# Kernel tuning notes

Measured on AMD Instinct MI355X. Metric: run time of the kernel, lower is better.

## Reference

```python
import jax, jax.numpy as jnp
import numpy as np


def setup_inputs() -> dict:
    key = jax.random.key(0)
    kH, kU, kW = jax.random.split(key, 3)
    T, J, D2 = 16384, 1024, 512  # T x 2d context, J x 2d query
    H = jax.random.normal(kH, (T, D2), dtype=jnp.float32)
    U = jax.random.normal(kU, (J, D2), dtype=jnp.float32)
    Ws = jax.random.normal(kW, (3 * D2, 1), dtype=jnp.float32) * 0.05
    return {"H": H, "U": U, "Ws": Ws}


def reference(H, U, Ws):
    D2 = H.shape[-1]
    # Ws applied to concat([H_dup, U_dup, H_dup*U_dup]) decomposes into three blocks.
    w1 = Ws[:D2, 0]          # (2d,)
    w2 = Ws[D2:2 * D2, 0]    # (2d,)
    w3 = Ws[2 * D2:, 0]      # (2d,)
    # Trilinear similarity S[t, j] = H[t]@w1 + U[j]@w2 + (H[t]*U[j])@w3  -> (T, J)
    S = (H @ w1)[:, None] + (U @ w2)[None, :] + (H * w3) @ U.T
    # C2Q attention: softmax over query axis, attend query vectors -> (T, 2d)
    attended_query = jax.nn.softmax(S, axis=-1) @ U
    # Q2C attention: softmax over T of max_j S, rank-1 summary of context -> (2d,)
    b = jax.nn.softmax(jnp.max(S, axis=-1))
    h_tilde = b @ H  # (2d,), tiled to (T, 2d) by broadcasting
    # Merge to query-aware representation G -> (T, 8d)
    G = jnp.concatenate(
        [H, attended_query, H * attended_query, H * h_tilde[None, :]], axis=-1
    )
    return G
```

## Files before the change

### kernel.cpp

```cpp
#include <hip/hip_runtime.h>
#include <hip/hip_bf16.h>

#define T_ROWS 16384
#define J_DIM  1024
#define D_DIM  512

typedef __attribute__((ext_vector_type(8))) short bf16x8;
typedef __attribute__((ext_vector_type(4))) float f32x4;
typedef unsigned short u16;

__device__ __forceinline__ u16 f2bf(float f) {
    union { float f; unsigned int u; } v; v.f = f;
    return (u16)((v.u + 0x7FFFu + ((v.u >> 16) & 1u)) >> 16);
}
__device__ __forceinline__ float bf2f(u16 b) {
    union { unsigned int u; float f; } v; v.u = ((unsigned int)b) << 16;
    return v.f;
}

__device__ __forceinline__ void gload16(const void* g, void* l) {
    __builtin_amdgcn_global_load_lds(
        (__attribute__((address_space(1))) void*)(unsigned long long)(size_t)g,
        (__attribute__((address_space(3))) void*)(unsigned int)(size_t)l,
        16, 0, 0);
}

template<int NT>
__device__ __forceinline__ void gemm_core(
    const u16* A, int lda, const u16* B, int ldb, u16* lds, f32x4 (&acc)[4][4])
{
    const int tid  = threadIdx.x;
    const int lane = tid & 63;
    const int w    = tid >> 6;
    const int wr   = w >> 1, wc = w & 1;
    const int fr   = lane & 15, quad = lane >> 4;

    const int srow = tid >> 2;
    const int ss   = (tid & 3) ^ ((srow >> 1) & 3);

    const u16* gA0 = A + (size_t)srow * lda + ss * 8;
    const u16* gA1 = A + (size_t)(srow + 64) * lda + ss * 8;
    const u16* gB0 = B + (size_t)srow * ldb + ss * 8;
    const u16* gB1 = B + (size_t)(srow + 64) * ldb + ss * 8;

    u16* As = lds;
    u16* Bs = lds + 8192;
    u16* dA0 = As + tid * 8;
    u16* dA1 = As + 2048 + tid * 8;
    u16* dB0 = Bs + tid * 8;
    u16* dB1 = Bs + 2048 + tid * 8;

    gload16(gA0, dA0); gload16(gA1, dA1);
    gload16(gB0, dB0); gload16(gB1, dB1);
    gA0 += 32; gA1 += 32; gB0 += 32; gB1 += 32;

    int offA[4], offB[4];
    #pragma unroll
    for (int i = 0; i < 4; ++i) {
        const int rA = wr * 64 + i * 16 + fr;
        offA[i] = rA * 32 + (quad ^ ((rA >> 1) & 3)) * 8;
        const int rB = wc * 64 + i * 16 + fr;
        offB[i] = rB * 32 + (quad ^ ((rB >> 1) & 3)) * 8;
    }
    __syncthreads();

    #pragma unroll 2
    for (int t = 0; t < NT; ++t) {
        const int cur = (t & 1) * 4096;
        const int nxt = 4096 - cur;
        if (t + 1 < NT) {
            gload16(gA0, dA0 + nxt); gload16(gA1, dA1 + nxt);
            gload16(gB0, dB0 + nxt); gload16(gB1, dB1 + nxt);
            gA0 += 32; gA1 += 32; gB0 += 32; gB1 += 32;
        }
        const u16* Ac = As + cur;
        const u16* Bc = Bs + cur;
        bf16x8 af[4], bfr[4];
        #pragma unroll
        for (int i = 0; i < 4; ++i) af[i]  = *(const bf16x8*)(Ac + offA[i]);
        #pragma unroll
        for (int i = 0; i < 4; ++i) bfr[i] = *(const bf16x8*)(Bc + offB[i]);
        #pragma unroll
        for (int mf = 0; mf < 4; ++mf)
            #pragma unroll
            for (int nf = 0; nf < 4; ++nf)
                acc[mf][nf] = __builtin_amdgcn_mfma_f32_16x16x32_bf16(
                    af[mf], bfr[nf], acc[mf][nf], 0, 0, 0);
        __syncthreads();
    }
}

__global__ __launch_bounds__(128) void prep_u(
    const float* __restrict__ U, const float* __restrict__ Ws,
    float* __restrict__ uw2, u16* __restrict__ Ub, u16* __restrict__ Utp)
{
    const int j = blockIdx.x;
    const int t = threadIdx.x;
    const float4 u  = ((const float4*)(U + (size_t)j * D_DIM))[t];
    const float4 w2 = ((const float4*)(Ws + D_DIM))[t];
    float p = u.x * w2.x + u.y * w2.y + u.z * w2.z + u.w * w2.w;
    #pragma unroll
    for (int m = 1; m < 64; m <<= 1) p += __shfl_xor(p, m);
    __shared__ float red[2];
    if ((t & 63) == 0) red[t >> 6] = p;
    __syncthreads();
    if (t == 0) uw2[j] = red[0] + red[1];

    ushort4 v;
    v.x = f2bf(u.x); v.y = f2bf(u.y); v.z = f2bf(u.z); v.w = f2bf(u.w);
    ((ushort4*)(Ub + (size_t)j * D_DIM))[t] = v;

    const size_t jpart = (size_t)(j >> 5) * 512 + (size_t)(((j >> 3) & 3) * 128) + (j & 7);
    const u16 bs[4] = { v.x, v.y, v.z, v.w };
    #pragma unroll
    for (int s = 0; s < 4; ++s) {
        const int d = 4 * t + s;
        Utp[(size_t)(d >> 4) * 16384 + jpart + (size_t)(d & 15) * 8] = bs[s];
    }
}

__global__ __launch_bounds__(128) void prep_h(
    const float* __restrict__ H, const float* __restrict__ Ws,
    float* __restrict__ hw1, u16* outU)
{
    const int i = blockIdx.x;
    const int t = threadIdx.x;
    const float4 h  = ((const float4*)(H + (size_t)i * D_DIM))[t];
    const float4 w1 = ((const float4*)Ws)[t];
    const float4 w3 = ((const float4*)(Ws + 2 * D_DIM))[t];
    float p = h.x * w1.x + h.y * w1.y + h.z * w1.z + h.w * w1.w;
    #pragma unroll
    for (int m = 1; m < 64; m <<= 1) p += __shfl_xor(p, m);
    __shared__ float red[2];
    if ((t & 63) == 0) red[t >> 6] = p;
    __syncthreads();
    if (t == 0) hw1[i] = red[0] + red[1];

    ushort4 q;
    q.x = f2bf(h.x * w3.x); q.y = f2bf(h.y * w3.y);
    q.z = f2bf(h.z * w3.z); q.w = f2bf(h.w * w3.w);
    *(ushort4*)(outU + (size_t)i * 4096 + 3072 + 4 * t) = q;
}

__global__ __launch_bounds__(256) void s_gemm(
    u16* outU, const u16* __restrict__ Ub, const float* __restrict__ uw2,
    float* __restrict__ pmax)
{
    __shared__ u16 lds[16384];
    const int bid = blockIdx.x;
    const int swz = (bid & 7) * 128 + (bid >> 3);
    const int bm = swz >> 3, nb = swz & 7;

    f32x4 acc[4][4];
    #pragma unroll
    for (int i = 0; i < 4; ++i)
        #pragma unroll
        for (int j = 0; j < 4; ++j) acc[i][j] = (f32x4){0.f, 0.f, 0.f, 0.f};

    gemm_core<16>(outU + (size_t)bm * 128 * 4096 + 3072, 4096,
                  Ub + (size_t)nb * 128 * 512, 512, lds, acc);

    const int tid = threadIdx.x, lane = tid & 63, w = tid >> 6;
    const int wr = w >> 1, wc = w & 1, fr = lane & 15, quad = lane >> 4;
    int jc[4]; float u2[4];
    #pragma unroll
    for (int nf = 0; nf < 4; ++nf) {
        jc[nf] = nb * 128 + wc * 64 + nf * 16 + fr;
        u2[nf] = uw2[jc[nf]];
    }
    float* redf = (float*)lds;
    #pragma unroll
    for (int mf = 0; mf < 4; ++mf)
        #pragma unroll
        for (int m = 0; m < 4; ++m) {
            float mv = -1e30f;
            #pragma unroll
            for (int nf = 0; nf < 4; ++nf) {
                acc[mf][nf][m] += u2[nf];
                mv = fmaxf(mv, acc[mf][nf][m]);
            }
            mv = fmaxf(mv, __shfl_xor(mv, 1));
            mv = fmaxf(mv, __shfl_xor(mv, 2));
            mv = fmaxf(mv, __shfl_xor(mv, 4));
            mv = fmaxf(mv, __shfl_xor(mv, 8));
            if (fr == 0) redf[wc * 128 + wr * 64 + mf * 16 + quad * 4 + m] = mv;
        }
    __syncthreads();
    if (wc == 0 && fr == 0) {
        #pragma unroll
        for (int mf = 0; mf < 4; ++mf)
            #pragma unroll
            for (int m = 0; m < 4; ++m) {
                const int rr = wr * 64 + mf * 16 + quad * 4 + m;
                pmax[((size_t)bm * 128 + rr) * 8 + nb] =
                    fmaxf(redf[rr], redf[128 + rr]);
            }
    }
    #pragma unroll
    for (int mf = 0; mf < 4; ++mf)
        #pragma unroll
        for (int m = 0; m < 4; ++m) {
            const size_t row = (size_t)bm * 128 + wr * 64 + mf * 16 + quad * 4 + m;
            u16* rp = outU + row * 4096 + 1024;
            #pragma unroll
            for (int nf = 0; nf < 4; ++nf) rp[jc[nf]] = f2bf(acc[mf][nf][m]);
        }
}

__global__ __launch_bounds__(1024) void bsoft2(
    const float* __restrict__ pmax, const float* __restrict__ hw1,
    float* __restrict__ bvec)
{
    __shared__ float red[16];
    __shared__ float Msh, Lsh;
    const int t = threadIdx.x;
    float rs[16];
    #pragma unroll
    for (int e = 0; e < 16; ++e) {
        const int r = t + e * 1024;
        const float4 p0 = *(const float4*)(pmax + (size_t)r * 8);
        const float4 p1 = *(const float4*)(pmax + (size_t)r * 8 + 4);
        rs[e] = fmaxf(fmaxf(fmaxf(p0.x, p0.y), fmaxf(p0.z, p0.w)),
                      fmaxf(fmaxf(p1.x, p1.y), fmaxf(p1.z, p1.w))) + hw1[r];
    }
    float m = -1e30f;
    #pragma unroll
    for (int e = 0; e < 16; ++e) m = fmaxf(m, rs[e]);
    #pragma unroll
    for (int s = 1; s < 64; s <<= 1) m = fmaxf(m, __shfl_xor(m, s));
    if ((t & 63) == 0) red[t >> 6] = m;
    __syncthreads();
    if (t == 0) {
        float M = red[0];
        for (int i = 1; i < 16; ++i) M = fmaxf(M, red[i]);
        Msh = M;
    }
    __syncthreads();
    const float M = Msh;
    float l = 0.f;
    #pragma unroll
    for (int e = 0; e < 16; ++e) l += __expf(rs[e] - M);
    #pragma unroll
    for (int s = 1; s < 64; s <<= 1) l += __shfl_xor(l, s);
    if ((t & 63) == 0) red[t >> 6] = l;
    __syncthreads();
    if (t == 0) {
        float L = 0.f;
        for (int i = 0; i < 16; ++i) L += red[i];
        Lsh = L;
    }
    __syncthreads();
    const float invL = 1.f / Lsh;
    #pragma unroll
    for (int e = 0; e < 16; ++e) bvec[t + e * 1024] = __expf(rs[e] - M) * invL;
}

__global__ __launch_bounds__(512) void htilde_partial(
    const float* __restrict__ H, const float* __restrict__ b,
    float* __restrict__ part)
{
    const int blk = blockIdx.x;
    const int d = threadIdx.x;
    const int i0 = blk * 64;
    float s = 0.f;
    for (int rI = 0; rI < 64; ++rI)
        s += b[i0 + rI] * H[(size_t)(i0 + rI) * D_DIM + d];
    part[(size_t)blk * D_DIM + d] = s;
}

__global__ __launch_bounds__(512) void htilde_reduce(
    const float* __restrict__ part, float* __restrict__ ht)
{
    const int d = threadIdx.x;
    float s = 0.f;
    for (int p = 0; p < 256; ++p) s += part[(size_t)p * D_DIM + d];
    ht[d] = s;
}

__global__ __launch_bounds__(512) void pv_fused(
    u16* outU, const u16* __restrict__ Utp, const float* __restrict__ H,
    const float* __restrict__ htld)
{
    __shared__ u16 SP[64 * 1024];
    const int tid = threadIdx.x, lane = tid & 63, w = tid >> 6;
    const int fr = lane & 15, quad = lane >> 4;
    const int ib = blockIdx.x * 64;

    {
        const int r_off = tid >> 7;
        const int c8 = tid & 127;
        #pragma unroll
        for (int p = 0; p < 16; ++p) {
            const int r = p * 4 + r_off;
            gload16(outU + (size_t)(ib + r) * 4096 + 1024 + (size_t)((c8 ^ (r & 7)) * 8),
                    SP + (size_t)p * 4096 + (size_t)tid * 8);
        }
    }
    __syncthreads();

    #pragma unroll
    for (int rr = 0; rr < 8; ++rr) {
        const int r = w * 8 + rr;
        u16* row = SP + (size_t)r * 1024;
        const int s0 = (lane ^ rr) * 8;
        const int s1 = ((lane + 64) ^ rr) * 8;
        bf16x8 x0 = *(bf16x8*)(row + s0);
        bf16x8 x1 = *(bf16x8*)(row + s1);
        float f0[8], f1[8];
        float mx = -1e30f;
        #pragma unroll
        for (int i = 0; i < 8; ++i) {
            f0[i] = bf2f((u16)x0[i]); f1[i] = bf2f((u16)x1[i]);
            mx = fmaxf(mx, fmaxf(f0[i], f1[i]));
        }
        #pragma unroll
        for (int s = 1; s < 64; s <<= 1) mx = fmaxf(mx, __shfl_xor(mx, s));
        float sum = 0.f;
        #pragma unroll
        for (int i = 0; i < 8; ++i) {
            f0[i] = __expf(f0[i] - mx); f1[i] = __expf(f1[i] - mx);
            sum += f0[i] + f1[i];
        }
        #pragma unroll
        for (int s = 1; s < 64; s <<= 1) sum += __shfl_xor(sum, s);
        const float inv = 1.f / sum;
        bf16x8 y0, y1;
        #pragma unroll
        for (int i = 0; i < 8; ++i) {
            y0[i] = (short)f2bf(f0[i] * inv);
            y1[i] = (short)f2bf(f1[i] * inv);
        }
        *(bf16x8*)(row + s0) = y0;
        *(bf16x8*)(row + s1) = y1;
    }
    __syncthreads();

    f32x4 acc[4][4];
    #pragma unroll
    for (int i = 0; i < 4; ++i)
        #pragma unroll
        for (int j = 0; j < 4; ++j) acc[i][j] = (f32x4){0.f, 0.f, 0.f, 0.f};

    const u16* bp = Utp + (size_t)lane * 8;
    bf16x8 bA[4], bB[4];
    #pragma unroll
    for (int nf = 0; nf < 4; ++nf)
        bA[nf] = *(const bf16x8*)(bp + ((size_t)(w * 4 + nf) * 32) * 512);

    for (int ks = 0; ks < 32; ks += 2) {
        #pragma unroll
        for (int nf = 0; nf < 4; ++nf)
            bB[nf] = *(const bf16x8*)(bp + ((size_t)(w * 4 + nf) * 32 + ks + 1) * 512);
        bf16x8 a0[4];
        #pragma unroll
        for (int mf = 0; mf < 4; ++mf)
            a0[mf] = *(const bf16x8*)(SP + (size_t)(mf * 16 + fr) * 1024
                                         + (size_t)(((ks * 4 + quad) ^ (fr & 7)) * 8));
        #pragma unroll
        for (int mf = 0; mf < 4; ++mf)
            #pragma unroll
            for (int nf = 0; nf < 4; ++nf)
                acc[mf][nf] = __builtin_amdgcn_mfma_f32_16x16x32_bf16(
                    a0[mf], bA[nf], acc[mf][nf], 0, 0, 0);
        if (ks + 2 < 32) {
            #pragma unroll
            for (int nf = 0; nf < 4; ++nf)
                bA[nf] = *(const bf16x8*)(bp + ((size_t)(w * 4 + nf) * 32 + ks + 2) * 512);
        }
        bf16x8 a1[4];
        #pragma unroll
        for (int mf = 0; mf < 4; ++mf)
            a1[mf] = *(const bf16x8*)(SP + (size_t)(mf * 16 + fr) * 1024
                                         + (size_t)((((ks + 1) * 4 + quad) ^ (fr & 7)) * 8));
        #pragma unroll
        for (int mf = 0; mf < 4; ++mf)
            #pragma unroll
            for (int nf = 0; nf < 4; ++nf)
                acc[mf][nf] = __builtin_amdgcn_mfma_f32_16x16x32_bf16(
                    a1[mf], bB[nf], acc[mf][nf], 0, 0, 0);
    }

    float ht[4];
    #pragma unroll
    for (int nf = 0; nf < 4; ++nf) ht[nf] = htld[w * 64 + nf * 16 + fr];
    #pragma unroll
    for (int mf = 0; mf < 4; ++mf)
        #pragma unroll
        for (int m = 0; m < 4; ++m) {
            const size_t row = (size_t)ib + mf * 16 + quad * 4 + m;
            const float* hrow = H + row * D_DIM;
            float* ob = (float*)outU + row * 2048;
            #pragma unroll
            for (int nf = 0; nf < 4; ++nf) {
                const int c = w * 64 + nf * 16 + fr;
                const float h  = hrow[c];
                const float aq = acc[mf][nf][m];
                ob[c]        = h;
                ob[512 + c]  = aq;
                ob[1024 + c] = h * aq;
                ob[1536 + c] = h * ht[nf];
            }
        }
}

extern "C" void kernel_launch(void* const* d_in, const int* in_sizes, int n_in,
                              void* d_out, int out_size, void* d_ws, size_t ws_size,
                              hipStream_t stream)
{
    const float* H  = (const float*)d_in[0];
    const float* U  = (const float*)d_in[1];
    const float* Ws = (const float*)d_in[2];
    u16* outU = (u16*)d_out;

    float* uw2   = (float*)d_ws;
    float* hw1   = uw2 + 1024;
    float* bvec  = hw1 + T_ROWS;
    float* htld  = bvec + T_ROWS;
    float* part  = htld + D_DIM;
    float* pmax  = part + 256 * D_DIM;
    u16*   Ub    = (u16*)(pmax + (size_t)T_ROWS * 8);
    u16*   Utp   = Ub + (size_t)J_DIM * D_DIM;

    hipLaunchKernelGGL(prep_u, dim3(J_DIM), dim3(128), 0, stream, U, Ws, uw2, Ub, Utp);
    hipLaunchKernelGGL(prep_h, dim3(T_ROWS), dim3(128), 0, stream, H, Ws, hw1, outU);
    hipLaunchKernelGGL(s_gemm, dim3(1024), dim3(256), 0, stream, outU, Ub, uw2, pmax);
    hipLaunchKernelGGL(bsoft2, dim3(1), dim3(1024), 0, stream, pmax, hw1, bvec);
    hipLaunchKernelGGL(htilde_partial, dim3(256), dim3(512), 0, stream, H, bvec, part);
    hipLaunchKernelGGL(htilde_reduce, dim3(1), dim3(512), 0, stream, part, htld);
    hipLaunchKernelGGL(pv_fused, dim3(T_ROWS / 64), dim3(512), 0, stream,
                       outU, Utp, H, htld);
}
```

Measured before the change: 130.8 us.

## Halve pv_fused row tile and stage outputs through LDS for float4 stores

pv_fused now handles 32 rows per block instead of 64. This cuts LDS from 128KB to about 65KB and doubles the grid to 512 blocks, so more blocks can be resident. The accumulators are written to a padded LDS tile and the epilogue then writes coalesced float4 rows of H, aq, H*aq and H*htilde, replacing the scattered scalar stores. The cost is that each Utp B-fragment is reused over fewer rows, so more B traffic per output, plus an extra LDS round trip and barriers.

```diff
diff --git a/kernel.cpp b/kernel.cpp
--- a/kernel.cpp
+++ b/kernel.cpp
@@ -277,33 +277,32 @@
     ht[d] = s;
 }
 
-__global__ __launch_bounds__(512) void pv_fused(
+__global__ __launch_bounds__(512, 4) void pv_fused(
     u16* outU, const u16* __restrict__ Utp, const float* __restrict__ H,
     const float* __restrict__ htld)
 {
-    __shared__ u16 SP[64 * 1024];
+    __shared__ float SPf[32 * 520];
+    u16* SP = (u16*)SPf;
     const int tid = threadIdx.x, lane = tid & 63, w = tid >> 6;
     const int fr = lane & 15, quad = lane >> 4;
-    const int ib = blockIdx.x * 64;
-
-    {
-        const int r_off = tid >> 7;
-        const int c8 = tid & 127;
-        #pragma unroll
-        for (int p = 0; p < 16; ++p) {
-            const int r = p * 4 + r_off;
-            gload16(outU + (size_t)(ib + r) * 4096 + 1024 + (size_t)((c8 ^ (r & 7)) * 8),
-                    SP + (size_t)p * 4096 + (size_t)tid * 8);
-        }
-    }
-    __syncthreads();
-
-    #pragma unroll
-    for (int rr = 0; rr < 8; ++rr) {
-        const int r = w * 8 + rr;
+    const int ib = blockIdx.x * 32;
+
+    #pragma unroll
+    for (int p = 0; p < 8; ++p) {
+        const int slot = p * 512 + tid;
+        const int r  = slot >> 7;
+        const int c8 = slot & 127;
+        gload16(outU + (size_t)(ib + r) * 4096 + 1024 + (size_t)((c8 ^ (r & 7)) * 8),
+                SP + (size_t)slot * 8);
+    }
+    __syncthreads();
+
+    #pragma unroll
+    for (int rr = 0; rr < 4; ++rr) {
+        const int r = w * 4 + rr;
         u16* row = SP + (size_t)r * 1024;
-        const int s0 = (lane ^ rr) * 8;
-        const int s1 = ((lane + 64) ^ rr) * 8;
+        const int s0 = (lane ^ (r & 7)) * 8;
+        const int s1 = ((lane + 64) ^ (r & 7)) * 8;
         bf16x8 x0 = *(bf16x8*)(row + s0);
         bf16x8 x1 = *(bf16x8*)(row + s1);
         float f0[8], f1[8];
@@ -335,9 +334,9 @@
     }
     __syncthreads();
 
-    f32x4 acc[4][4];
-    #pragma unroll
-    for (int i = 0; i < 4; ++i)
+    f32x4 acc[2][4];
+    #pragma unroll
+    for (int i = 0; i < 2; ++i)
         #pragma unroll
         for (int j = 0; j < 4; ++j) acc[i][j] = (f32x4){0.f, 0.f, 0.f, 0.f};
 
@@ -351,13 +350,13 @@
         #pragma unroll
         for (int nf = 0; nf < 4; ++nf)
             bB[nf] = *(const bf16x8*)(bp + ((size_t)(w * 4 + nf) * 32 + ks + 1) * 512);
-        bf16x8 a0[4];
-        #pragma unroll
-        for (int mf = 0; mf < 4; ++mf)
+        bf16x8 a0[2];
+        #pragma unroll
+        for (int mf = 0; mf < 2; ++mf)
             a0[mf] = *(const bf16x8*)(SP + (size_t)(mf * 16 + fr) * 1024
                                          + (size_t)(((ks * 4 + quad) ^ (fr & 7)) * 8));
         #pragma unroll
-        for (int mf = 0; mf < 4; ++mf)
+        for (int mf = 0; mf < 2; ++mf)
             #pragma unroll
             for (int nf = 0; nf < 4; ++nf)
                 acc[mf][nf] = __builtin_amdgcn_mfma_f32_16x16x32_bf16(
@@ -367,40 +366,52 @@
             for (int nf = 0; nf < 4; ++nf)
                 bA[nf] = *(const bf16x8*)(bp + ((size_t)(w * 4 + nf) * 32 + ks + 2) * 512);
         }
-        bf16x8 a1[4];
-        #pragma unroll
-        for (int mf = 0; mf < 4; ++mf)
+        bf16x8 a1[2];
+        #pragma unroll
+        for (int mf = 0; mf < 2; ++mf)
             a1[mf] = *(const bf16x8*)(SP + (size_t)(mf * 16 + fr) * 1024
                                          + (size_t)((((ks + 1) * 4 + quad) ^ (fr & 7)) * 8));
         #pragma unroll
-        for (int mf = 0; mf < 4; ++mf)
+        for (int mf = 0; mf < 2; ++mf)
             #pragma unroll
             for (int nf = 0; nf < 4; ++nf)
                 acc[mf][nf] = __builtin_amdgcn_mfma_f32_16x16x32_bf16(
                     a1[mf], bB[nf], acc[mf][nf], 0, 0, 0);
     }
-
-    float ht[4];
-    #pragma unroll
-    for (int nf = 0; nf < 4; ++nf) ht[nf] = htld[w * 64 + nf * 16 + fr];
-    #pragma unroll
-    for (int mf = 0; mf < 4; ++mf)
+    __syncthreads();
+
+    #pragma unroll
+    for (int mf = 0; mf < 2; ++mf)
         #pragma unroll
         for (int m = 0; m < 4; ++m) {
-            const size_t row = (size_t)ib + mf * 16 + quad * 4 + m;
-            const float* hrow = H + row * D_DIM;
-            float* ob = (float*)outU + row * 2048;
-            #pragma unroll
-            for (int nf = 0; nf < 4; ++nf) {
-                const int c = w * 64 + nf * 16 + fr;
-                const float h  = hrow[c];
-                const float aq = acc[mf][nf][m];
-                ob[c]        = h;
-                ob[512 + c]  = aq;
-                ob[1024 + c] = h * aq;
-                ob[1536 + c] = h * ht[nf];
-            }
-        }
+            const int r = mf * 16 + quad * 4 + m;
+            #pragma unroll
+            for (int nf = 0; nf < 4; ++nf)
+                SPf[r * 520 + w * 64 + nf * 16 + fr] = acc[mf][nf][m];
+        }
+    __syncthreads();
+
+    {
+        const int r = tid >> 4;
+        const int l16 = tid & 15;
+        const size_t grow = (size_t)ib + r;
+        const float* hrow = H + grow * D_DIM;
+        float* ob = (float*)outU + grow * 2048;
+        #pragma unroll
+        for (int i = 0; i < 8; ++i) {
+            const int c = l16 * 4 + i * 64;
+            const float4 h  = *(const float4*)(hrow + c);
+            const float4 aq = *(const float4*)(&SPf[r * 520 + c]);
+            const float4 hv = *(const float4*)(htld + c);
+            float4 ha, hh;
+            ha.x = h.x * aq.x; ha.y = h.y * aq.y; ha.z = h.z * aq.z; ha.w = h.w * aq.w;
+            hh.x = h.x * hv.x; hh.y = h.y * hv.y; hh.z = h.z * hv.z; hh.w = h.w * hv.w;
+            *(float4*)(ob + c)        = h;
+            *(float4*)(ob + 512 + c)  = aq;
+            *(float4*)(ob + 1024 + c) = ha;
+            *(float4*)(ob + 1536 + c) = hh;
+        }
+    }
 }
 
 extern "C" void kernel_launch(void* const* d_in, const int* in_sizes, int n_in,
@@ -427,6 +438,6 @@
     hipLaunchKernelGGL(bsoft2, dim3(1), dim3(1024), 0, stream, pmax, hw1, bvec);
     hipLaunchKernelGGL(htilde_partial, dim3(256), dim3(512), 0, stream, H, bvec, part);
     hipLaunchKernelGGL(htilde_reduce, dim3(1), dim3(512), 0, stream, part, htld);
-    hipLaunchKernelGGL(pv_fused, dim3(T_ROWS / 64), dim3(512), 0, stream,
+    hipLaunchKernelGGL(pv_fused, dim3(T_ROWS / 32), dim3(512), 0, stream,
                        outU, Utp, H, htld);
 }
```

Result: no change. 132.9 us (+1.6%).
